# Optimization experiments

Hardware: AMD Instinct MI355X
Metric: run time of the kernel (lower is better)

Reference implementation:

```python
import jax, jax.numpy as jnp
import numpy as np

N = 50000
E = 800000
IN_DIM = 128
OUT_DIM = 128
EDGE_DIM = 3
H = 4
HD = OUT_DIM // H  # 32
SCALE = HD ** -0.5


def setup_inputs() -> dict:
    key = jax.random.key(0)
    ks = jax.random.split(key, 10)
    x = jax.random.normal(ks[0], (N, IN_DIM), dtype=jnp.float32)
    edge_index = jax.random.randint(ks[1], (2, E), 0, N, dtype=jnp.int64)
    edge_attr = jax.random.normal(ks[2], (E, EDGE_DIM), dtype=jnp.float32)
    s = 1.0 / np.sqrt(IN_DIM)
    Wq = jax.random.normal(ks[3], (IN_DIM, H * HD), dtype=jnp.float32) * s
    Wk = jax.random.normal(ks[4], (IN_DIM, H * HD), dtype=jnp.float32) * s
    Wv = jax.random.normal(ks[5], (IN_DIM, H * HD), dtype=jnp.float32) * s
    We = jax.random.normal(ks[6], (EDGE_DIM, H), dtype=jnp.float32) * (1.0 / np.sqrt(EDGE_DIM))
    Wo = jax.random.normal(ks[7], (H * HD, OUT_DIM), dtype=jnp.float32) * (1.0 / np.sqrt(H * HD))
    bo = jnp.zeros((OUT_DIM,), dtype=jnp.float32)
    Wm = jax.random.normal(ks[8], (IN_DIM + OUT_DIM, OUT_DIM), dtype=jnp.float32) * (1.0 / np.sqrt(IN_DIM + OUT_DIM))
    bm = jnp.zeros((OUT_DIM,), dtype=jnp.float32)
    return {"x": x, "edge_index": edge_index, "edge_attr": edge_attr,
            "Wq": Wq, "Wk": Wk, "Wv": Wv, "We": We, "Wo": Wo, "bo": bo,
            "Wm": Wm, "bm": bm}


def reference(x, edge_index, edge_attr, Wq, Wk, Wv, We, Wo, bo, Wm, bm):
    n = x.shape[0]
    src = edge_index[0]
    dst = edge_index[1]
    Q = (x @ Wq).reshape(n, H, HD)
    K = (x @ Wk).reshape(n, H, HD)
    V = (x @ Wv).reshape(n, H, HD)
    edge_bias = edge_attr @ We                                  # [E, H]
    attn = jnp.sum(Q[dst] * K[src], axis=-1) * SCALE + edge_bias  # [E, H]
    attn = jnp.where(attn >= 0, attn, 0.2 * attn)               # leaky_relu(0.2)
    # NOTE: original uses a single GLOBAL max over all edges/heads for stability
    attn_exp = jnp.exp(attn - jnp.max(attn))
    attn_sum = jax.ops.segment_sum(attn_exp, dst, num_segments=n)  # [N, H]
    attn_norm = attn_exp / jnp.maximum(attn_sum[dst], 1e-12)
    # dropout disabled (eval mode)
    weighted_V = V[src] * attn_norm[:, :, None]                 # [E, H, HD]
    agg = jax.ops.segment_sum(weighted_V, dst, num_segments=n)  # [N, H, HD]
    agg = agg.reshape(n, H * HD) @ Wo + bo                      # [N, OUT]
    h = jnp.concatenate([x, agg], axis=1) @ Wm + bm
    return jax.nn.relu(h)
```

## Files before the change

### kernel.cpp

```cpp
#include <hip/hip_runtime.h>
#include <hip/hip_bf16.h>
#include <math.h>

#define NN 50000
#define NE 800000
#define DIM 128
#define NH 4
#define HD 32
#define ATTN_SCALE 0.17677669529663687f
#define MTILE 64
#define GEMM_BLOCKS 782
#define NBKT 98
#define PTS 2048
#define HBLKS 104

#define PREP_QKV_BASE  104
#define PREP_WXB_BASE  296
#define PREP_X_BASE    361
#define PREP_GRID      6611

#define PQ_PART_N   391
#define PQ_QKV_BASE 391
#define PQ_PACKO_BASE 1173
#define PQ_GRID     1301

typedef unsigned int uint;
typedef unsigned short ushort;
typedef __attribute__((ext_vector_type(8))) short short8;
typedef __attribute__((ext_vector_type(4))) float f32x4;

__device__ inline ushort f2bf(float f) {
    __hip_bfloat16 h = __float2bfloat16(f);
    return *(ushort*)&h;
}
__device__ inline float bflo(uint u) { return __uint_as_float(u << 16); }
__device__ inline float bfhi(uint u) { return __uint_as_float(u & 0xffff0000u); }
__device__ inline float bf2f(ushort u) { return __uint_as_float((uint)u << 16); }

__global__ __launch_bounds__(256) void prep_all_kernel(
    const float* __restrict__ x, ushort* __restrict__ xb,
    const int* __restrict__ dst, int* __restrict__ bkt_cnt,
    const float* __restrict__ Wq, const float* __restrict__ Wk,
    const float* __restrict__ Wv, short* __restrict__ BpQKV,
    const float* __restrict__ Wo, const float* __restrict__ Wm,
    const float* __restrict__ bo, const float* __restrict__ bm,
    float* __restrict__ Wx, float* __restrict__ bprime)
{
    const int bid = blockIdx.x;
    const int tid = threadIdx.x;

    if (bid < PREP_QKV_BASE) {
        __shared__ int c[NBKT];
        if (tid < NBKT) c[tid] = 0;
        __syncthreads();
        for (int e = bid * 256 + tid; e < NE; e += HBLKS * 256)
            atomicAdd(&c[dst[e] >> 9], 1);
        __syncthreads();
        if (tid < NBKT && c[tid]) atomicAdd(&bkt_cnt[tid], c[tid]);
    } else if (bid < PREP_WXB_BASE) {
        const int idx = (bid - PREP_QKV_BASE) * 256 + tid;
        const int j = idx & 7, lane = (idx >> 3) & 63;
        const int rest = idx >> 9;
        const int nt = rest % 24, kc = rest / 24;
        const int k = kc * 32 + (lane >> 4) * 8 + j;
        const int n = nt * 16 + (lane & 15);
        const float* W = (n < 128) ? Wq : (n < 256 ? Wk : Wv);
        BpQKV[idx] = (short)f2bf(W[k * 128 + (n & 127)]);
    } else if (bid < PREP_X_BASE) {
        const int r = (bid - PREP_WXB_BASE) * 2 + (tid >> 7);
        const int j = tid & 127;
        if (r < 128) {
            float acc = 0.f;
            for (int t = 0; t < 128; ++t)
                acc = fmaf(Wo[r * 128 + t], Wm[(128 + t) * 128 + j], acc);
            Wx[r * 128 + j] = acc;
        } else if (r == 128) {
            float acc = bm[j];
            for (int t = 0; t < 128; ++t)
                acc = fmaf(bo[t], Wm[(128 + t) * 128 + j], acc);
            bprime[j] = acc;
        }
    } else {
        const int i = (bid - PREP_X_BASE) * 256 + tid;
        const float4 v = ((const float4*)x)[i];
        ushort4 o;
        o.x = f2bf(v.x); o.y = f2bf(v.y); o.z = f2bf(v.z); o.w = f2bf(v.w);
        ((ushort4*)xb)[i] = o;
    }
}

__global__ void bkt_scan_kernel(const int* __restrict__ bkt_cnt,
                                int* __restrict__ bkt_base,
                                int* __restrict__ bkt_cursor,
                                int* __restrict__ rowptr)
{
    if (threadIdx.x == 0) {
        int run = 0;
        for (int b = 0; b < NBKT; ++b) {
            bkt_base[b] = run;
            bkt_cursor[b] = run;
            run += bkt_cnt[b];
        }
        bkt_base[NBKT] = run;
        rowptr[NN] = run;
    }
}

__global__ __launch_bounds__(256) void partqkv_kernel(
    const int* __restrict__ src, const int* __restrict__ dst,
    const float* __restrict__ edge_attr, const float* __restrict__ We,
    int* __restrict__ bkt_cursor,
    uint* __restrict__ ppack, uint2* __restrict__ pebp,
    const ushort* __restrict__ xb, const short* __restrict__ BpQKV,
    ushort* __restrict__ Qb, ushort* __restrict__ Kb, ushort* __restrict__ Vb,
    const float* __restrict__ Wm, const float* __restrict__ Wx,
    short* __restrict__ BpOut)
{
    const int bid = blockIdx.x;
    const int tid = threadIdx.x;

    if (bid < PQ_PART_N) {
        __shared__ int cnt[NBKT], rbase[NBKT], cnt2[NBKT];
        if (tid < NBKT) cnt[tid] = 0;
        __syncthreads();
        const int e0 = bid * PTS;
        #pragma unroll
        for (int it = 0; it < 8; ++it) {
            const int e = e0 + it * 256 + tid;
            if (e < NE) atomicAdd(&cnt[dst[e] >> 9], 1);
        }
        __syncthreads();
        if (tid < NBKT) {
            rbase[tid] = cnt[tid] ? atomicAdd(&bkt_cursor[tid], cnt[tid]) : 0;
            cnt2[tid] = 0;
        }
        __syncthreads();
        #pragma unroll
        for (int it = 0; it < 8; ++it) {
            const int e = e0 + it * 256 + tid;
            if (e < NE) {
                const int d = dst[e];
                const int b = d >> 9;
                const int r = atomicAdd(&cnt2[b], 1);
                const int pos = rbase[b] + r;
                ppack[pos] = (uint)src[e] | ((uint)(d & 511) << 16);
                const float a0 = edge_attr[e * 3 + 0];
                const float a1 = edge_attr[e * 3 + 1];
                const float a2 = edge_attr[e * 3 + 2];
                const float b0 = a0 * We[0] + a1 * We[4] + a2 * We[8];
                const float b1 = a0 * We[1] + a1 * We[5] + a2 * We[9];
                const float b2 = a0 * We[2] + a1 * We[6] + a2 * We[10];
                const float b3 = a0 * We[3] + a1 * We[7] + a2 * We[11];
                uint2 ep;
                ep.x = (uint)f2bf(b0) | ((uint)f2bf(b1) << 16);
                ep.y = (uint)f2bf(b2) | ((uint)f2bf(b3) << 16);
                pebp[pos] = ep;
            }
        }
    } else if (bid < PQ_PACKO_BASE) {
        const int qb = bid - PQ_QKV_BASE;
        const int wave = tid >> 6;
        const int lane = tid & 63;
        const int m = lane & 15, quad = lane >> 4;
        const int row0w = qb * MTILE + wave * 16;
        const int arow = row0w + m;
        const bool rowok = arow < NN;

        short8 a[4];
        #pragma unroll
        for (int kc = 0; kc < 4; ++kc)
            a[kc] = rowok ? *(const short8*)(xb + (size_t)arow * 128 + kc * 32 + quad * 8)
                          : (short8)(0);

        const int NT = 24;
        for (int nt = 0; nt < NT; nt += 2) {
            f32x4 acc0 = {0.f, 0.f, 0.f, 0.f}, acc1 = {0.f, 0.f, 0.f, 0.f};
            #pragma unroll
            for (int kc = 0; kc < 4; ++kc) {
                const short8 b0 = *(const short8*)(BpQKV + ((size_t)(kc * NT + nt) * 64 + lane) * 8);
                const short8 b1 = *(const short8*)(BpQKV + ((size_t)(kc * NT + nt + 1) * 64 + lane) * 8);
                acc0 = __builtin_amdgcn_mfma_f32_16x16x32_bf16(a[kc], b0, acc0, 0, 0, 0);
                acc1 = __builtin_amdgcn_mfma_f32_16x16x32_bf16(a[kc], b1, acc1, 0, 0, 0);
            }
            #pragma unroll
            for (int t = 0; t < 2; ++t) {
                const f32x4 acc = t ? acc1 : acc0;
                const int c = (nt + t) * 16 + m;
                ushort* dstp_ = (c < 128) ? Qb : (c < 256 ? Kb : Vb);
                const int lc = c & 127;
                #pragma unroll
                for (int g = 0; g < 4; ++g) {
                    const int r = row0w + quad * 4 + g;
                    if (r < NN) dstp_[(size_t)r * 128 + lc] = f2bf(acc[g]);
                }
            }
        }
    } else {
        const int idx = (bid - PQ_PACKO_BASE) * 256 + tid;
        const int j = idx & 7, lane = (idx >> 3) & 63;
        const int rest = idx >> 9;
        const int nt = rest & 7, kc = rest >> 3;
        const int k = kc * 32 + (lane >> 4) * 8 + j;
        const int n = nt * 16 + (lane & 15);
        const float v = (k < 128) ? Wm[k * 128 + n] : Wx[(k - 128) * 128 + n];
        BpOut[idx] = (short)f2bf(v);
    }
}

__global__ __launch_bounds__(256) void bucket_csr_kernel(
    const int* __restrict__ bkt_base,
    const uint* __restrict__ ppack, const uint2* __restrict__ pebp,
    int* __restrict__ rowptr,
    ushort* __restrict__ srcp, uint2* __restrict__ ebq)
{
    __shared__ int cnt[512];
    __shared__ int pre[512];
    __shared__ int sc[256];
    const int tid = threadIdx.x;
    const int b = blockIdx.x;
    const int base = bkt_base[b];
    const int n = bkt_base[b + 1] - base;
    const int node0 = b << 9;

    cnt[tid] = 0; cnt[tid + 256] = 0;
    __syncthreads();
    for (int i = base + tid; i < base + n; i += 256)
        atomicAdd(&cnt[ppack[i] >> 16], 1);
    __syncthreads();

    const int pair = cnt[2 * tid] + cnt[2 * tid + 1];
    sc[tid] = pair;
    __syncthreads();
    for (int off = 1; off < 256; off <<= 1) {
        const int v = (tid >= off) ? sc[tid - off] : 0;
        __syncthreads();
        sc[tid] += v;
        __syncthreads();
    }
    const int ex = sc[tid] - pair;
    pre[2 * tid] = base + ex;
    pre[2 * tid + 1] = base + ex + cnt[2 * tid];
    __syncthreads();

    for (int l = tid; l < 512; l += 256) {
        const int g = node0 + l;
        if (g < NN) rowptr[g] = pre[l];
    }
    __syncthreads();

    for (int i = base + tid; i < base + n; i += 256) {
        const uint v = ppack[i];
        const int pos = atomicAdd(&pre[v >> 16], 1);
        srcp[pos] = (ushort)(v & 0xFFFFu);
        ebq[pos] = pebp[i];
    }
}

__global__ __launch_bounds__(256) void out_mfma_kernel(
    const ushort* __restrict__ xb, const ushort* __restrict__ aggb,
    const short* __restrict__ Bp, const float* __restrict__ bprime,
    float* __restrict__ out)
{
    const int wave = threadIdx.x >> 6;
    const int lane = threadIdx.x & 63;
    const int m = lane & 15, quad = lane >> 4;
    const int row0w = blockIdx.x * MTILE + wave * 16;
    const int arow = row0w + m;
    const bool rowok = arow < NN;

    short8 a[8];
    #pragma unroll
    for (int kc = 0; kc < 4; ++kc)
        a[kc] = rowok ? *(const short8*)(xb + (size_t)arow * 128 + kc * 32 + quad * 8)
                      : (short8)(0);
    #pragma unroll
    for (int kc = 0; kc < 4; ++kc)
        a[4 + kc] = rowok ? *(const short8*)(aggb + (size_t)arow * 128 + kc * 32 + quad * 8)
                          : (short8)(0);

    const int NT = 8;
    for (int nt = 0; nt < NT; nt += 2) {
        f32x4 acc0 = {0.f, 0.f, 0.f, 0.f}, acc1 = {0.f, 0.f, 0.f, 0.f};
        #pragma unroll
        for (int kc = 0; kc < 8; ++kc) {
            const short8 b0 = *(const short8*)(Bp + ((size_t)(kc * NT + nt) * 64 + lane) * 8);
            const short8 b1 = *(const short8*)(Bp + ((size_t)(kc * NT + nt + 1) * 64 + lane) * 8);
            acc0 = __builtin_amdgcn_mfma_f32_16x16x32_bf16(a[kc], b0, acc0, 0, 0, 0);
            acc1 = __builtin_amdgcn_mfma_f32_16x16x32_bf16(a[kc], b1, acc1, 0, 0, 0);
        }
        #pragma unroll
        for (int t = 0; t < 2; ++t) {
            const f32x4 acc = t ? acc1 : acc0;
            const int c = (nt + t) * 16 + m;
            const float bb = bprime[c];
            #pragma unroll
            for (int g = 0; g < 4; ++g) {
                const int r = row0w + quad * 4 + g;
                if (r < NN) out[(size_t)r * 128 + c] = fmaxf(acc[g] + bb, 0.f);
            }
        }
    }
}

__global__ __launch_bounds__(256) void attn_agg_kernel(
    const ushort* __restrict__ Qb, const ushort* __restrict__ Kb,
    const ushort* __restrict__ Vb,
    const int* __restrict__ rowptr, const ushort* __restrict__ srcp,
    const ushort* __restrict__ ebb, ushort* __restrict__ aggb)
{
    const int tid = threadIdx.x;
    const int d = blockIdx.x * 4 + (tid >> 6);
    const int lane = tid & 63;
    const int g = lane >> 4;
    const int t = lane & 15;
    const int h = t >> 2;
    const int begin = rowptr[d];
    const int end   = rowptr[d + 1];

    const uint4 uq = *(const uint4*)(Qb + (size_t)d * DIM + 8 * t);
    const float q0 = bflo(uq.x), q1 = bfhi(uq.x);
    const float q2 = bflo(uq.y), q3 = bfhi(uq.y);
    const float q4 = bflo(uq.z), q5 = bfhi(uq.z);
    const float q6 = bflo(uq.w), q7 = bfhi(uq.w);

    float ss = 0.f;
    float a0 = 0.f, a1 = 0.f, a2 = 0.f, a3 = 0.f;
    float a4 = 0.f, a5 = 0.f, a6 = 0.f, a7 = 0.f;

    if (begin < end) {
        int ec = begin + g;
        if (ec >= end) ec = end - 1;
        int s    = (int)srcp[ec];
        float eb = bf2f(ebb[ec * 4 + h]);

        for (int p = begin; p < end; p += 4) {
            const bool ok = (p + g) < end;
            const int pn = p + 4;
            int sn = s; float ebn = eb;
            if (pn < end) {
                int en = pn + g;
                if (en >= end) en = end - 1;
                sn  = (int)srcp[en];
                ebn = bf2f(ebb[en * 4 + h]);
            }

            const uint4 uk = *(const uint4*)(Kb + (size_t)s * DIM + 8 * t);
            const uint4 uv = *(const uint4*)(Vb + (size_t)s * DIM + 8 * t);

            float da = q0 * bflo(uk.x);
            float db = q1 * bfhi(uk.x);
            da = fmaf(q2, bflo(uk.y), da);
            db = fmaf(q3, bfhi(uk.y), db);
            da = fmaf(q4, bflo(uk.z), da);
            db = fmaf(q5, bfhi(uk.z), db);
            da = fmaf(q6, bflo(uk.w), da);
            db = fmaf(q7, bfhi(uk.w), db);
            float part = da + db;
            part += __shfl_xor(part, 1);
            part += __shfl_xor(part, 2);

            float a = fmaf(part, ATTN_SCALE, eb);
            a = (a >= 0.f) ? a : 0.2f * a;
            float w = ok ? __expf(a) : 0.f;

            ss += w;
            a0 = fmaf(w, bflo(uv.x), a0);
            a1 = fmaf(w, bfhi(uv.x), a1);
            a2 = fmaf(w, bflo(uv.y), a2);
            a3 = fmaf(w, bfhi(uv.y), a3);
            a4 = fmaf(w, bflo(uv.z), a4);
            a5 = fmaf(w, bfhi(uv.z), a5);
            a6 = fmaf(w, bflo(uv.w), a6);
            a7 = fmaf(w, bfhi(uv.w), a7);

            s = sn; eb = ebn;
        }
    }

    ss += __shfl_xor(ss, 16);
    ss += __shfl_xor(ss, 32);
    a0 += __shfl_xor(a0, 16); a0 += __shfl_xor(a0, 32);
    a1 += __shfl_xor(a1, 16); a1 += __shfl_xor(a1, 32);
    a2 += __shfl_xor(a2, 16); a2 += __shfl_xor(a2, 32);
    a3 += __shfl_xor(a3, 16); a3 += __shfl_xor(a3, 32);
    a4 += __shfl_xor(a4, 16); a4 += __shfl_xor(a4, 32);
    a5 += __shfl_xor(a5, 16); a5 += __shfl_xor(a5, 32);
    a6 += __shfl_xor(a6, 16); a6 += __shfl_xor(a6, 32);
    a7 += __shfl_xor(a7, 16); a7 += __shfl_xor(a7, 32);

    if (g == 0) {
        const float inv = 1.f / fmaxf(ss, 1e-12f);
        uint4 o;
        o.x = (uint)f2bf(a0 * inv) | ((uint)f2bf(a1 * inv) << 16);
        o.y = (uint)f2bf(a2 * inv) | ((uint)f2bf(a3 * inv) << 16);
        o.z = (uint)f2bf(a4 * inv) | ((uint)f2bf(a5 * inv) << 16);
        o.w = (uint)f2bf(a6 * inv) | ((uint)f2bf(a7 * inv) << 16);
        *(uint4*)(aggb + (size_t)d * DIM + 8 * t) = o;
    }
}

extern "C" void kernel_launch(void* const* d_in, const int* in_sizes, int n_in,
                              void* d_out, int out_size, void* d_ws, size_t ws_size,
                              hipStream_t stream)
{
    const float* x         = (const float*)d_in[0];
    const int*   edge_idx  = (const int*)d_in[1];
    const float* edge_attr = (const float*)d_in[2];
    const float* Wq        = (const float*)d_in[3];
    const float* Wk        = (const float*)d_in[4];
    const float* Wv        = (const float*)d_in[5];
    const float* We        = (const float*)d_in[6];
    const float* Wo        = (const float*)d_in[7];
    const float* bo        = (const float*)d_in[8];
    const float* Wm        = (const float*)d_in[9];
    const float* bm        = (const float*)d_in[10];
    float* out = (float*)d_out;

    const int* src = edge_idx;
    const int* dst = edge_idx + NE;

    ushort* xb   = (ushort*)d_ws;
    ushort* Qb   = xb + (size_t)NN * DIM;
    ushort* Kb   = Qb + (size_t)NN * DIM;
    ushort* Vb   = Kb + (size_t)NN * DIM;
    ushort* aggb = Vb + (size_t)NN * DIM;
    uint*  ppack = (uint*)(aggb + (size_t)NN * DIM);
    uint2* pebp  = (uint2*)(ppack + NE);
    uint2* ebq   = pebp + NE;
    ushort* srcp = (ushort*)(ebq + NE);
    float* Wx    = (float*)(srcp + NE);
    float* bprime= Wx + 16384;
    short* BpQKV = (short*)(bprime + 128);
    short* BpOut = BpQKV + 49152;
    int*   rowptr= (int*)(BpOut + 32768);
    int*   bkt_cnt    = rowptr + 50048;
    int*   bkt_base   = bkt_cnt + 128;
    int*   bkt_cursor = bkt_base + 128;

    hipMemsetAsync(bkt_cnt, 0, 128 * sizeof(int), stream);

    prep_all_kernel<<<PREP_GRID, 256, 0, stream>>>(
        x, xb, dst, bkt_cnt, Wq, Wk, Wv, BpQKV, Wo, Wm, bo, bm, Wx, bprime);

    bkt_scan_kernel<<<1, 64, 0, stream>>>(bkt_cnt, bkt_base, bkt_cursor, rowptr);

    partqkv_kernel<<<PQ_GRID, 256, 0, stream>>>(
        src, dst, edge_attr, We, bkt_cursor, ppack, pebp,
        xb, BpQKV, Qb, Kb, Vb, Wm, Wx, BpOut);

    bucket_csr_kernel<<<NBKT, 256, 0, stream>>>(bkt_base, ppack, pebp,
                                                rowptr, srcp, ebq);

    attn_agg_kernel<<<NN / 4, 256, 0, stream>>>(Qb, Kb, Vb, rowptr, srcp,
                                                (const ushort*)ebq, aggb);

    out_mfma_kernel<<<GEMM_BLOCKS, 256, 0, stream>>>(xb, aggb, BpOut, bprime, out);
}
```

Baseline: 254.1 us.

## Move QKV GEMM into CSR kernel, split buckets, interleave K and V rows

Restructures the launch schedule. The QKV GEMM blocks now run in the same launch as the CSR build instead of alongside partitioning. The CSR step is split into 8 sub-blocks per bucket, 782 in all, so it parallelises beyond 98 blocks. K and V are stored interleaved per node so the gather touches one contiguous 512-byte row. The cost is that each sub-block re-reads and re-scans its whole bucket, an 8x redundant histogram and scan.

```diff
diff --git a/kernel.cpp b/kernel.cpp
--- a/kernel.cpp
+++ b/kernel.cpp
@@ -19,10 +19,11 @@
 #define PREP_X_BASE    361
 #define PREP_GRID      6611
 
-#define PQ_PART_N   391
-#define PQ_QKV_BASE 391
-#define PQ_PACKO_BASE 1173
-#define PQ_GRID     1301
+#define PART_N      391
+#define PART_GRID   519
+
+#define CSR_N       782
+#define CSRQ_GRID   1564
 
 typedef unsigned int uint;
 typedef unsigned short ushort;
@@ -106,20 +107,18 @@
     }
 }
 
-__global__ __launch_bounds__(256) void partqkv_kernel(
+__global__ __launch_bounds__(256) void part_kernel(
     const int* __restrict__ src, const int* __restrict__ dst,
     const float* __restrict__ edge_attr, const float* __restrict__ We,
     int* __restrict__ bkt_cursor,
     uint* __restrict__ ppack, uint2* __restrict__ pebp,
-    const ushort* __restrict__ xb, const short* __restrict__ BpQKV,
-    ushort* __restrict__ Qb, ushort* __restrict__ Kb, ushort* __restrict__ Vb,
     const float* __restrict__ Wm, const float* __restrict__ Wx,
     short* __restrict__ BpOut)
 {
     const int bid = blockIdx.x;
     const int tid = threadIdx.x;
 
-    if (bid < PQ_PART_N) {
+    if (bid < PART_N) {
         __shared__ int cnt[NBKT], rbase[NBKT], cnt2[NBKT];
         if (tid < NBKT) cnt[tid] = 0;
         __syncthreads();
@@ -157,8 +156,77 @@
                 pebp[pos] = ep;
             }
         }
-    } else if (bid < PQ_PACKO_BASE) {
-        const int qb = bid - PQ_QKV_BASE;
+    } else {
+        const int idx = (bid - PART_N) * 256 + tid;
+        const int j = idx & 7, lane = (idx >> 3) & 63;
+        const int rest = idx >> 9;
+        const int nt = rest & 7, kc = rest >> 3;
+        const int k = kc * 32 + (lane >> 4) * 8 + j;
+        const int n = nt * 16 + (lane & 15);
+        const float v = (k < 128) ? Wm[k * 128 + n] : Wx[(k - 128) * 128 + n];
+        BpOut[idx] = (short)f2bf(v);
+    }
+}
+
+__global__ __launch_bounds__(256) void csrqkv_kernel(
+    const int* __restrict__ bkt_base,
+    const uint* __restrict__ ppack, const uint2* __restrict__ pebp,
+    int* __restrict__ rowptr,
+    ushort* __restrict__ srcp, uint2* __restrict__ ebq,
+    const ushort* __restrict__ xb, const short* __restrict__ BpQKV,
+    ushort* __restrict__ Qb, ushort* __restrict__ KVb)
+{
+    const int bid = blockIdx.x;
+    const int tid = threadIdx.x;
+
+    if (bid < CSR_N) {
+        __shared__ int cnt[512];
+        __shared__ int pre[512];
+        __shared__ int sc[256];
+        const int parent = bid >> 3;
+        const int sub    = bid & 7;
+        const int base = bkt_base[parent];
+        const int n = bkt_base[parent + 1] - base;
+        const int node0 = parent << 9;
+
+        cnt[tid] = 0; cnt[tid + 256] = 0;
+        __syncthreads();
+        for (int i = base + tid; i < base + n; i += 256)
+            atomicAdd(&cnt[ppack[i] >> 16], 1);
+        __syncthreads();
+
+        const int pair = cnt[2 * tid] + cnt[2 * tid + 1];
+        sc[tid] = pair;
+        __syncthreads();
+        for (int off = 1; off < 256; off <<= 1) {
+            const int v = (tid >= off) ? sc[tid - off] : 0;
+            __syncthreads();
+            sc[tid] += v;
+            __syncthreads();
+        }
+        const int ex = sc[tid] - pair;
+        pre[2 * tid] = base + ex;
+        pre[2 * tid + 1] = base + ex + cnt[2 * tid];
+        __syncthreads();
+
+        if (tid < 64) {
+            const int l = sub * 64 + tid;
+            const int g = node0 + l;
+            if (g < NN) rowptr[g] = pre[l];
+        }
+        __syncthreads();
+
+        for (int i = base + tid; i < base + n; i += 256) {
+            const uint v = ppack[i];
+            const int l = v >> 16;
+            if ((l >> 6) == sub) {
+                const int pos = atomicAdd(&pre[l], 1);
+                srcp[pos] = (ushort)(v & 0xFFFFu);
+                ebq[pos] = pebp[i];
+            }
+        }
+    } else {
+        const int qb = bid - CSR_N;
         const int wave = tid >> 6;
         const int lane = tid & 63;
         const int m = lane & 15, quad = lane >> 4;
@@ -186,73 +254,16 @@
             for (int t = 0; t < 2; ++t) {
                 const f32x4 acc = t ? acc1 : acc0;
                 const int c = (nt + t) * 16 + m;
-                ushort* dstp_ = (c < 128) ? Qb : (c < 256 ? Kb : Vb);
-                const int lc = c & 127;
                 #pragma unroll
                 for (int g = 0; g < 4; ++g) {
                     const int r = row0w + quad * 4 + g;
-                    if (r < NN) dstp_[(size_t)r * 128 + lc] = f2bf(acc[g]);
+                    if (r < NN) {
+                        if (c < 128) Qb[(size_t)r * 128 + c] = f2bf(acc[g]);
+                        else        KVb[(size_t)r * 256 + (c - 128)] = f2bf(acc[g]);
+                    }
                 }
             }
         }
-    } else {
-        const int idx = (bid - PQ_PACKO_BASE) * 256 + tid;
-        const int j = idx & 7, lane = (idx >> 3) & 63;
-        const int rest = idx >> 9;
-        const int nt = rest & 7, kc = rest >> 3;
-        const int k = kc * 32 + (lane >> 4) * 8 + j;
-        const int n = nt * 16 + (lane & 15);
-        const float v = (k < 128) ? Wm[k * 128 + n] : Wx[(k - 128) * 128 + n];
-        BpOut[idx] = (short)f2bf(v);
-    }
-}
-
-__global__ __launch_bounds__(256) void bucket_csr_kernel(
-    const int* __restrict__ bkt_base,
-    const uint* __restrict__ ppack, const uint2* __restrict__ pebp,
-    int* __restrict__ rowptr,
-    ushort* __restrict__ srcp, uint2* __restrict__ ebq)
-{
-    __shared__ int cnt[512];
-    __shared__ int pre[512];
-    __shared__ int sc[256];
-    const int tid = threadIdx.x;
-    const int b = blockIdx.x;
-    const int base = bkt_base[b];
-    const int n = bkt_base[b + 1] - base;
-    const int node0 = b << 9;
-
-    cnt[tid] = 0; cnt[tid + 256] = 0;
-    __syncthreads();
-    for (int i = base + tid; i < base + n; i += 256)
-        atomicAdd(&cnt[ppack[i] >> 16], 1);
-    __syncthreads();
-
-    const int pair = cnt[2 * tid] + cnt[2 * tid + 1];
-    sc[tid] = pair;
-    __syncthreads();
-    for (int off = 1; off < 256; off <<= 1) {
-        const int v = (tid >= off) ? sc[tid - off] : 0;
-        __syncthreads();
-        sc[tid] += v;
-        __syncthreads();
-    }
-    const int ex = sc[tid] - pair;
-    pre[2 * tid] = base + ex;
-    pre[2 * tid + 1] = base + ex + cnt[2 * tid];
-    __syncthreads();
-
-    for (int l = tid; l < 512; l += 256) {
-        const int g = node0 + l;
-        if (g < NN) rowptr[g] = pre[l];
-    }
-    __syncthreads();
-
-    for (int i = base + tid; i < base + n; i += 256) {
-        const uint v = ppack[i];
-        const int pos = atomicAdd(&pre[v >> 16], 1);
-        srcp[pos] = (ushort)(v & 0xFFFFu);
-        ebq[pos] = pebp[i];
     }
 }
 
@@ -303,8 +314,7 @@
 }
 
 __global__ __launch_bounds__(256) void attn_agg_kernel(
-    const ushort* __restrict__ Qb, const ushort* __restrict__ Kb,
-    const ushort* __restrict__ Vb,
+    const ushort* __restrict__ Qb, const ushort* __restrict__ KVb,
     const int* __restrict__ rowptr, const ushort* __restrict__ srcp,
     const ushort* __restrict__ ebb, ushort* __restrict__ aggb)
 {
@@ -344,8 +354,9 @@
                 ebn = bf2f(ebb[en * 4 + h]);
             }
 
-            const uint4 uk = *(const uint4*)(Kb + (size_t)s * DIM + 8 * t);
-            const uint4 uv = *(const uint4*)(Vb + (size_t)s * DIM + 8 * t);
+            const ushort* kv = KVb + (size_t)s * 256 + 8 * t;
+            const uint4 uk = *(const uint4*)(kv);
+            const uint4 uv = *(const uint4*)(kv + 128);
 
             float da = q0 * bflo(uk.x);
             float db = q1 * bfhi(uk.x);
@@ -421,9 +432,8 @@
 
     ushort* xb   = (ushort*)d_ws;
     ushort* Qb   = xb + (size_t)NN * DIM;
-    ushort* Kb   = Qb + (size_t)NN * DIM;
-    ushort* Vb   = Kb + (size_t)NN * DIM;
-    ushort* aggb = Vb + (size_t)NN * DIM;
+    ushort* KVb  = Qb + (size_t)NN * DIM;
+    ushort* aggb = KVb + (size_t)NN * 2 * DIM;
     uint*  ppack = (uint*)(aggb + (size_t)NN * DIM);
     uint2* pebp  = (uint2*)(ppack + NE);
     uint2* ebq   = pebp + NE;
@@ -444,14 +454,13 @@
 
     bkt_scan_kernel<<<1, 64, 0, stream>>>(bkt_cnt, bkt_base, bkt_cursor, rowptr);
 
-    partqkv_kernel<<<PQ_GRID, 256, 0, stream>>>(
-        src, dst, edge_attr, We, bkt_cursor, ppack, pebp,
-        xb, BpQKV, Qb, Kb, Vb, Wm, Wx, BpOut);
-
-    bucket_csr_kernel<<<NBKT, 256, 0, stream>>>(bkt_base, ppack, pebp,
-                                                rowptr, srcp, ebq);
-
-    attn_agg_kernel<<<NN / 4, 256, 0, stream>>>(Qb, Kb, Vb, rowptr, srcp,
+    part_kernel<<<PART_GRID, 256, 0, stream>>>(
+        src, dst, edge_attr, We, bkt_cursor, ppack, pebp, Wm, Wx, BpOut);
+
+    csrqkv_kernel<<<CSRQ_GRID, 256, 0, stream>>>(
+        bkt_base, ppack, pebp, rowptr, srcp, ebq, xb, BpQKV, Qb, KVb);
+
+    attn_agg_kernel<<<NN / 4, 256, 0, stream>>>(Qb, KVb, rowptr, srcp,
                                                 (const ushort*)ebq, aggb);
 
     out_mfma_kernel<<<GEMM_BLOCKS, 256, 0, stream>>>(xb, aggb, BpOut, bprime, out);
```

After: 249.3 us. Within noise of the previous version (-1.9%).
